# Kernel optimization log

Measured on AMD Instinct MI355X. Metric: run time of the kernel, lower is better.

The kernel has to match this reference:

```python
import jax, jax.numpy as jnp
import numpy as np

EMBED_DIM = 2048
EPS = 1e-6
B, L, H, D = 4, 4096, 16, 128


def setup_inputs() -> dict:
    key = jax.random.key(0)
    k1, k2, k3, k4, k5 = jax.random.split(key, 5)
    return {
        "Q": jax.random.normal(k1, (B, L, H, D), dtype=jnp.float32),
        "K": jax.random.normal(k2, (B, L, H, D), dtype=jnp.float32),
        "V": jax.random.normal(k3, (B, L, H, D), dtype=jnp.float32),
        "phi_Q": jax.random.uniform(k4, (B, L, H, D), dtype=jnp.float32),
        "phi_K": jax.random.uniform(k5, (B, L, H, D), dtype=jnp.float32),
    }


def reference(Q, K, V, phi_Q, phi_K):
    b, l, h, d = Q.shape
    # global query: mean over sequence, scaled by 1/sqrt(embed_dim) -> [B,1,H,D]
    q_global = jnp.mean(Q, axis=1, keepdims=True) / jnp.sqrt(jnp.float32(EMBED_DIM))
    # RALA rescaling: softmax over sequence positions, scaled by L -> [B,1,H,L]
    alpha = jax.nn.softmax(jnp.einsum("bihd,blhd->bihl", q_global, K), axis=-1) * l
    # [B,1,H,L] -> [B,L,H,1]
    alpha_r = jnp.transpose(alpha[:, 0], (0, 2, 1))[..., None]
    phi_K_scaled = phi_K * alpha_r  # [B,L,H,D]
    K_sum = jnp.sum(phi_K_scaled, axis=1)  # [B,H,D]
    KV = jnp.einsum("blhd,blhe->bhde", phi_K_scaled, V)  # [B,H,D,D]
    numerator = jnp.einsum("blhd,bhde->blhe", phi_Q, KV)  # [B,L,H,D]
    denominator = jnp.einsum("blhd,bhd->blh", phi_Q, K_sum)[..., None] + EPS
    return numerator / denominator
```

## Files before the change

kernel.cpp:

```cpp
#include <hip/hip_runtime.h>
#include <cstdint>
#include <cstddef>

#define B_ 4
#define L_ 4096
#define H_ 16
#define D_ 128
#define HD_ (H_*D_)
#define LHD_ ((size_t)L_*HD_)
#define BH_ (B_*H_)
#define EPS_ 1e-6f

typedef float f32x4 __attribute__((ext_vector_type(4)));
typedef unsigned int u32x4 __attribute__((ext_vector_type(4)));
typedef short s16x8 __attribute__((ext_vector_type(8)));

__device__ __forceinline__ unsigned short f2bf(float f){
  unsigned int u = __float_as_uint(f);
  u += 0x7fffu + ((u >> 16) & 1u);
  return (unsigned short)(u >> 16);
}
__device__ __forceinline__ unsigned int pack2(float lo, float hi){
  return (unsigned int)f2bf(lo) | ((unsigned int)f2bf(hi) << 16);
}

__global__ __launch_bounds__(256) void k_qmean(const float* __restrict__ Q, float* __restrict__ qg){
  int b  = blockIdx.x >> 6;
  int l0 = (blockIdx.x & 63) * 64;
  const float* base = Q + (size_t)b * LHD_ + (size_t)l0 * HD_;
  int t = threadIdx.x;
  f32x4 a0 = {0.f,0.f,0.f,0.f}, a1 = {0.f,0.f,0.f,0.f};
  #pragma unroll 4
  for (int l = 0; l < 64; ++l){
    const f32x4* row = (const f32x4*)(base + (size_t)l * HD_);
    a0 += row[t];
    a1 += row[t + 256];
  }
  const float scale = 1.0f / (4096.0f * 45.254833995939045f);
  float* dst = qg + b * HD_;
  #pragma unroll
  for (int i = 0; i < 4; ++i){
    atomicAdd(dst + 4*t + i,        a0[i] * scale);
    atomicAdd(dst + 1024 + 4*t + i, a1[i] * scale);
  }
}

__global__ __launch_bounds__(256) void k_scores(const float* __restrict__ K, const float* __restrict__ qg,
                                                float* __restrict__ scores){
  int b  = blockIdx.x >> 6;
  int l0 = (blockIdx.x & 63) * 64;
  int t = threadIdx.x;
  int wave = t >> 6, lane = t & 63;
  f32x4 q[8];
  const f32x4* qv = (const f32x4*)(qg + b * HD_);
  #pragma unroll
  for (int j = 0; j < 8; ++j)
    q[j] = qv[(2*j + (lane >> 5)) * 32 + (lane & 31)];
  for (int li = wave; li < 64; li += 4){
    const f32x4* kv = (const f32x4*)(K + (size_t)b * LHD_ + (size_t)(l0 + li) * HD_);
    float s[8];
    #pragma unroll
    for (int j = 0; j < 8; ++j){
      f32x4 x = kv[j * 64 + lane];
      s[j] = x[0]*q[j][0] + x[1]*q[j][1] + x[2]*q[j][2] + x[3]*q[j][3];
    }
    #pragma unroll
    for (int off = 1; off < 32; off <<= 1){
      #pragma unroll
      for (int j = 0; j < 8; ++j) s[j] += __shfl_xor(s[j], off);
    }
    if ((lane & 31) == 0){
      int hb = lane >> 5;
      #pragma unroll
      for (int j = 0; j < 8; ++j)
        scores[(size_t)(b * H_ + 2*j + hb) * L_ + l0 + li] = s[j];
    }
  }
}

__global__ __launch_bounds__(256) void k_softmax(float* __restrict__ scores){
  int bh = blockIdx.x;
  float* s = scores + (size_t)bh * L_;
  int t = threadIdx.x;
  int wave = t >> 6, lane = t & 63;
  float v[16];
  #pragma unroll
  for (int j = 0; j < 16; ++j) v[j] = s[t + 256*j];
  float m = -1e30f;
  #pragma unroll
  for (int j = 0; j < 16; ++j) m = fmaxf(m, v[j]);
  #pragma unroll
  for (int off = 1; off < 64; off <<= 1) m = fmaxf(m, __shfl_xor(m, off));
  __shared__ float red[8];
  if (lane == 0) red[wave] = m;
  __syncthreads();
  m = fmaxf(fmaxf(red[0], red[1]), fmaxf(red[2], red[3]));
  float z = 0.f;
  #pragma unroll
  for (int j = 0; j < 16; ++j) z += __expf(v[j] - m);
  #pragma unroll
  for (int off = 1; off < 64; off <<= 1) z += __shfl_xor(z, off);
  if (lane == 0) red[4 + wave] = z;
  __syncthreads();
  z = red[4] + red[5] + red[6] + red[7];
  float scale = (float)L_ / z;
  #pragma unroll
  for (int j = 0; j < 16; ++j) s[t + 256*j] = __expf(v[j] - m) * scale;
}

__global__ __launch_bounds__(256) void k_kv(const float* __restrict__ phiK, const float* __restrict__ V,
                                            const float* __restrict__ alpha,
                                            float* __restrict__ KV_part, float* __restrict__ Ksum){
  int c  = blockIdx.x & 3;
  int bh = blockIdx.x >> 2;
  int b = bh >> 4, h = bh & 15;
  __shared__ unsigned int Al[128 * 20];
  __shared__ unsigned int Bl[128 * 20];
  __shared__ float ksred[128 * 8];
  int t = threadIdx.x;
  int wave = t >> 6, lane = t & 63, q = lane >> 4, r = lane & 15;
  int d4 = t & 31, lp = t >> 5;
  f32x4 acc[2][8];
  #pragma unroll
  for (int mt = 0; mt < 2; ++mt)
    #pragma unroll
    for (int nt = 0; nt < 8; ++nt){ f32x4 z = {0.f,0.f,0.f,0.f}; acc[mt][nt] = z; }
  float ksl[4] = {0.f,0.f,0.f,0.f};

  for (int kt = 0; kt < 32; ++kt){
    int lbase = c * 1024 + kt * 32;
    f32x4 xa[2][2], xb[2][2];
    float al[2][2];
    #pragma unroll
    for (int p = 0; p < 2; ++p){
      int gl = lbase + 16*p + 2*lp;
      const float* rowK = phiK + (((size_t)b * L_ + gl) * H_ + h) * D_;
      const float* rowV = V    + (((size_t)b * L_ + gl) * H_ + h) * D_;
      xa[p][0] = ((const f32x4*)rowK)[d4];
      xa[p][1] = ((const f32x4*)(rowK + HD_))[d4];
      xb[p][0] = ((const f32x4*)rowV)[d4];
      xb[p][1] = ((const f32x4*)(rowV + HD_))[d4];
      al[p][0] = alpha[(size_t)bh * L_ + gl];
      al[p][1] = alpha[(size_t)bh * L_ + gl + 1];
    }
    __syncthreads();
    #pragma unroll
    for (int p = 0; p < 2; ++p){
      int cw = 8*p + lp;
      int cg = cw >> 2, cl = cw & 3;
      int grp = 4 * (cg ^ (d4 & 3)) + cl;
      #pragma unroll
      for (int i = 0; i < 4; ++i){
        int d = 4*d4 + i;
        float w0 = xa[p][0][i] * al[p][0];
        float w1 = xa[p][1][i] * al[p][1];
        ksl[i] += w0 + w1;
        Al[d * 20 + grp] = pack2(w0, w1);
        Bl[d * 20 + grp] = pack2(xb[p][0][i], xb[p][1][i]);
      }
    }
    __syncthreads();
    s16x8 af[2], bf[8];
    #pragma unroll
    for (int mt = 0; mt < 2; ++mt){
      int m = 32*wave + 16*mt + r;
      af[mt] = *((const s16x8*)&Al[m * 20 + 4 * (q ^ ((m >> 2) & 3))]);
    }
    #pragma unroll
    for (int nt = 0; nt < 8; ++nt){
      int n = 16*nt + r;
      bf[nt] = *((const s16x8*)&Bl[n * 20 + 4 * (q ^ ((n >> 2) & 3))]);
    }
    #pragma unroll
    for (int mt = 0; mt < 2; ++mt)
      #pragma unroll
      for (int nt = 0; nt < 8; ++nt)
        acc[mt][nt] = __builtin_amdgcn_mfma_f32_16x16x32_bf16(af[mt], bf[nt], acc[mt][nt], 0, 0, 0);
  }

  size_t pb = ((size_t)c * BH_ + bh) * ((size_t)D_ * D_);
  #pragma unroll
  for (int mt = 0; mt < 2; ++mt)
    #pragma unroll
    for (int reg = 0; reg < 4; ++reg){
      int d = 32*wave + 16*mt + 4*q + reg;
      float* dst = KV_part + pb + (size_t)d * D_;
      #pragma unroll
      for (int nt = 0; nt < 8; ++nt)
        dst[16*nt + r] = acc[mt][nt][reg];
    }
  #pragma unroll
  for (int i = 0; i < 4; ++i) ksred[(4*d4 + i) * 8 + lp] = ksl[i];
  __syncthreads();
  if (t < 128){
    float s = 0.f;
    #pragma unroll
    for (int j = 0; j < 8; ++j) s += ksred[t * 8 + j];
    atomicAdd(Ksum + (size_t)bh * D_ + t, s);
  }
}

__global__ __launch_bounds__(256) void k_reduce(const float* __restrict__ KV_part, const float* __restrict__ Ksum,
                                                unsigned int* __restrict__ KVT, unsigned int* __restrict__ KsumT){
  int bh = blockIdx.x;
  int t = threadIdx.x;
  __shared__ float T[128 * 129];
  #pragma unroll 2
  for (int p = 0; p < 64; ++p){
    int idx = p * 256 + t;
    float s = KV_part[((size_t)0 * BH_ + bh) * 16384 + idx]
            + KV_part[((size_t)1 * BH_ + bh) * 16384 + idx]
            + KV_part[((size_t)2 * BH_ + bh) * 16384 + idx]
            + KV_part[((size_t)3 * BH_ + bh) * 16384 + idx];
    int d = idx >> 7, e = idx & 127;
    T[d * 129 + e] = s;
  }
  __syncthreads();
  #pragma unroll 2
  for (int p = 0; p < 32; ++p){
    int o2 = p * 256 + t;
    int e = o2 >> 6, d0 = (o2 & 63) * 2;
    KVT[(size_t)bh * 8192 + o2] = pack2(T[d0 * 129 + e], T[(d0 + 1) * 129 + e]);
  }
  if (t < 64)
    KsumT[(size_t)bh * 64 + t] = pack2(Ksum[(size_t)bh * 128 + 2*t], Ksum[(size_t)bh * 128 + 2*t + 1]);
}

__global__ __launch_bounds__(256) void k_out(const float* __restrict__ phiQ,
                                             const unsigned int* __restrict__ KVT,
                                             const unsigned int* __restrict__ KsumT,
                                             float* __restrict__ out){
  int chunk = blockIdx.x & 31;
  int bh = blockIdx.x >> 5;
  int b = bh >> 4, h = bh & 15;
  int l0 = chunk * 128;
  __shared__ __align__(16) unsigned short BT[144 * 136];
  int t = threadIdx.x;
  const u32x4* src = (const u32x4*)(KVT + (size_t)bh * 8192);
  #pragma unroll
  for (int p = 0; p < 8; ++p){
    int i = p * 256 + t;
    int row = i >> 4;
    int col = (i & 15) * 8;
    *((u32x4*)&BT[row * 136 + col]) = src[i];
  }
  if (t < 16) *((u32x4*)&BT[128 * 136 + t * 8]) = ((const u32x4*)(KsumT + (size_t)bh * 64))[t];
  if (t < 255){ u32x4 z = {0u,0u,0u,0u}; *((u32x4*)&BT[129 * 136 + t * 8]) = z; }
  __syncthreads();

  int wave = t >> 6, lane = t & 63, q = lane >> 4, r = lane & 15;
  f32x4 accN[2][8], accD[2];
  #pragma unroll
  for (int mt = 0; mt < 2; ++mt){
    f32x4 z = {0.f,0.f,0.f,0.f};
    accD[mt] = z;
    #pragma unroll
    for (int nt = 0; nt < 8; ++nt) accN[mt][nt] = z;
  }
  const float* A0 = phiQ + (((size_t)b * L_ + (l0 + 32*wave + r)) * H_ + h) * D_ + q * 8;
  const float* A1 = A0 + (size_t)16 * HD_;
  #pragma unroll
  for (int ks = 0; ks < 4; ++ks){
    s16x8 af[2];
    #pragma unroll
    for (int mt = 0; mt < 2; ++mt){
      const float* ap = (mt ? A1 : A0) + 32 * ks;
      f32x4 x0 = *((const f32x4*)ap);
      f32x4 x1 = *((const f32x4*)(ap + 4));
      union { s16x8 s; unsigned int u[4]; } fr;
      fr.u[0] = pack2(x0[0], x0[1]);
      fr.u[1] = pack2(x0[2], x0[3]);
      fr.u[2] = pack2(x1[0], x1[1]);
      fr.u[3] = pack2(x1[2], x1[3]);
      af[mt] = fr.s;
    }
    #pragma unroll
    for (int nt = 0; nt < 9; ++nt){
      int n = 16*nt + r;
      s16x8 bf = *((const s16x8*)&BT[n * 136 + q * 8 + 32 * ks]);
      if (nt < 8){
        accN[0][nt] = __builtin_amdgcn_mfma_f32_16x16x32_bf16(af[0], bf, accN[0][nt], 0, 0, 0);
        accN[1][nt] = __builtin_amdgcn_mfma_f32_16x16x32_bf16(af[1], bf, accN[1][nt], 0, 0, 0);
      } else {
        accD[0] = __builtin_amdgcn_mfma_f32_16x16x32_bf16(af[0], bf, accD[0], 0, 0, 0);
        accD[1] = __builtin_amdgcn_mfma_f32_16x16x32_bf16(af[1], bf, accD[1], 0, 0, 0);
      }
    }
  }
  #pragma unroll
  for (int mt = 0; mt < 2; ++mt)
    #pragma unroll
    for (int reg = 0; reg < 4; ++reg){
      float den = __shfl(accD[mt][reg], (lane & 48)) + EPS_;
      float inv = 1.0f / den;
      int l = l0 + 32*wave + 16*mt + 4*q + reg;
      float* orow = out + (((size_t)b * L_ + l) * H_ + h) * D_;
      #pragma unroll
      for (int nt = 0; nt < 8; ++nt)
        orow[16*nt + r] = accN[mt][nt][reg] * inv;
    }
}

extern "C" void kernel_launch(void* const* d_in, const int* in_sizes, int n_in,
                              void* d_out, int out_size, void* d_ws, size_t ws_size,
                              hipStream_t stream){
  const float* Q    = (const float*)d_in[0];
  const float* K    = (const float*)d_in[1];
  const float* V    = (const float*)d_in[2];
  const float* phiQ = (const float*)d_in[3];
  const float* phiK = (const float*)d_in[4];
  float* out = (float*)d_out;
  char* ws = (char*)d_ws;
  float* qg      = (float*)(ws);
  float* Ksum    = (float*)(ws + 32768);
  float* scores  = (float*)(ws + 65536);
  float* KV_part = (float*)(ws + 1114112);
  unsigned int* KVT   = (unsigned int*)(ws + 17891328);
  unsigned int* KsumT = (unsigned int*)(ws + 19988480);

  hipMemsetAsync(qg, 0, 65536, stream);
  k_qmean  <<<256,  256, 0, stream>>>(Q, qg);
  k_scores <<<256,  256, 0, stream>>>(K, qg, scores);
  k_softmax<<<64,   256, 0, stream>>>(scores);
  k_kv     <<<256,  256, 0, stream>>>(phiK, V, scores, KV_part, Ksum);
  k_reduce <<<64,   256, 0, stream>>>(KV_part, Ksum, KVT, KsumT);
  k_out    <<<2048, 256, 0, stream>>>(phiQ, KVT, KsumT, out);
}
```

Baseline: 620.5 us.

## Raise parallelism across qmean, scores, kv and reduce kernels with prefetching

k_qmean and k_scores now launch more blocks, each covering fewer sequence rows. k_kv moves to 512 threads per block, one M-tile per wave, and register-prefetches the next phiK/V tile while the current one is staged in shared memory. k_reduce splits each head's transpose across four blocks and uses vectorized loads. The aim is better occupancy and latency hiding on memory-bound stages, at the cost of more atomics in qmean and more per-block overhead. The trivial accN index change in k_out has no effect.

```diff
diff --git a/kernel.cpp b/kernel.cpp
--- a/kernel.cpp
+++ b/kernel.cpp
@@ -25,13 +25,13 @@
 }
 
 __global__ __launch_bounds__(256) void k_qmean(const float* __restrict__ Q, float* __restrict__ qg){
-  int b  = blockIdx.x >> 6;
-  int l0 = (blockIdx.x & 63) * 64;
+  int b  = blockIdx.x >> 7;
+  int l0 = (blockIdx.x & 127) * 32;
   const float* base = Q + (size_t)b * LHD_ + (size_t)l0 * HD_;
   int t = threadIdx.x;
   f32x4 a0 = {0.f,0.f,0.f,0.f}, a1 = {0.f,0.f,0.f,0.f};
   #pragma unroll 4
-  for (int l = 0; l < 64; ++l){
+  for (int l = 0; l < 32; ++l){
     const f32x4* row = (const f32x4*)(base + (size_t)l * HD_);
     a0 += row[t];
     a1 += row[t + 256];
@@ -47,8 +47,8 @@
 
 __global__ __launch_bounds__(256) void k_scores(const float* __restrict__ K, const float* __restrict__ qg,
                                                 float* __restrict__ scores){
-  int b  = blockIdx.x >> 6;
-  int l0 = (blockIdx.x & 63) * 64;
+  int b  = blockIdx.x >> 8;
+  int l0 = (blockIdx.x & 255) * 16;
   int t = threadIdx.x;
   int wave = t >> 6, lane = t & 63;
   f32x4 q[8];
@@ -56,7 +56,7 @@
   #pragma unroll
   for (int j = 0; j < 8; ++j)
     q[j] = qv[(2*j + (lane >> 5)) * 32 + (lane & 31)];
-  for (int li = wave; li < 64; li += 4){
+  for (int li = wave; li < 16; li += 4){
     const f32x4* kv = (const f32x4*)(K + (size_t)b * LHD_ + (size_t)(l0 + li) * HD_);
     float s[8];
     #pragma unroll
@@ -108,7 +108,7 @@
   for (int j = 0; j < 16; ++j) s[t + 256*j] = __expf(v[j] - m) * scale;
 }
 
-__global__ __launch_bounds__(256) void k_kv(const float* __restrict__ phiK, const float* __restrict__ V,
+__global__ __launch_bounds__(512) void k_kv(const float* __restrict__ phiK, const float* __restrict__ V,
                                             const float* __restrict__ alpha,
                                             float* __restrict__ KV_part, float* __restrict__ Ksum){
   int c  = blockIdx.x & 3;
@@ -116,113 +116,115 @@
   int b = bh >> 4, h = bh & 15;
   __shared__ unsigned int Al[128 * 20];
   __shared__ unsigned int Bl[128 * 20];
-  __shared__ float ksred[128 * 8];
+  __shared__ float ksred[128 * 16];
   int t = threadIdx.x;
   int wave = t >> 6, lane = t & 63, q = lane >> 4, r = lane & 15;
   int d4 = t & 31, lp = t >> 5;
-  f32x4 acc[2][8];
-  #pragma unroll
-  for (int mt = 0; mt < 2; ++mt)
-    #pragma unroll
-    for (int nt = 0; nt < 8; ++nt){ f32x4 z = {0.f,0.f,0.f,0.f}; acc[mt][nt] = z; }
+  f32x4 acc[8];
+  #pragma unroll
+  for (int nt = 0; nt < 8; ++nt){ f32x4 z = {0.f,0.f,0.f,0.f}; acc[nt] = z; }
   float ksl[4] = {0.f,0.f,0.f,0.f};
 
+  const size_t arow = (size_t)bh * L_;
+  int gl = c * 1024 + 2 * lp;
+  const float* rowK = phiK + (((size_t)b * L_ + gl) * H_ + h) * D_;
+  const float* rowV = V    + (((size_t)b * L_ + gl) * H_ + h) * D_;
+  f32x4 xa0 = ((const f32x4*)rowK)[d4];
+  f32x4 xa1 = ((const f32x4*)(rowK + HD_))[d4];
+  f32x4 xb0 = ((const f32x4*)rowV)[d4];
+  f32x4 xb1 = ((const f32x4*)(rowV + HD_))[d4];
+  float al0 = alpha[arow + gl];
+  float al1 = alpha[arow + gl + 1];
+
+  int cg = lp >> 2, cl = lp & 3;
+  int grp = 4 * (cg ^ (d4 & 3)) + cl;
+
   for (int kt = 0; kt < 32; ++kt){
-    int lbase = c * 1024 + kt * 32;
-    f32x4 xa[2][2], xb[2][2];
-    float al[2][2];
-    #pragma unroll
-    for (int p = 0; p < 2; ++p){
-      int gl = lbase + 16*p + 2*lp;
-      const float* rowK = phiK + (((size_t)b * L_ + gl) * H_ + h) * D_;
-      const float* rowV = V    + (((size_t)b * L_ + gl) * H_ + h) * D_;
-      xa[p][0] = ((const f32x4*)rowK)[d4];
-      xa[p][1] = ((const f32x4*)(rowK + HD_))[d4];
-      xb[p][0] = ((const f32x4*)rowV)[d4];
-      xb[p][1] = ((const f32x4*)(rowV + HD_))[d4];
-      al[p][0] = alpha[(size_t)bh * L_ + gl];
-      al[p][1] = alpha[(size_t)bh * L_ + gl + 1];
-    }
     __syncthreads();
     #pragma unroll
-    for (int p = 0; p < 2; ++p){
-      int cw = 8*p + lp;
-      int cg = cw >> 2, cl = cw & 3;
-      int grp = 4 * (cg ^ (d4 & 3)) + cl;
-      #pragma unroll
-      for (int i = 0; i < 4; ++i){
-        int d = 4*d4 + i;
-        float w0 = xa[p][0][i] * al[p][0];
-        float w1 = xa[p][1][i] * al[p][1];
-        ksl[i] += w0 + w1;
-        Al[d * 20 + grp] = pack2(w0, w1);
-        Bl[d * 20 + grp] = pack2(xb[p][0][i], xb[p][1][i]);
-      }
+    for (int i = 0; i < 4; ++i){
+      int d = 4*d4 + i;
+      float w0 = xa0[i] * al0;
+      float w1 = xa1[i] * al1;
+      ksl[i] += w0 + w1;
+      Al[d * 20 + grp] = pack2(w0, w1);
+      Bl[d * 20 + grp] = pack2(xb0[i], xb1[i]);
+    }
+    if (kt < 31){
+      int gl2 = c * 1024 + (kt + 1) * 32 + 2 * lp;
+      const float* nK = phiK + (((size_t)b * L_ + gl2) * H_ + h) * D_;
+      const float* nV = V    + (((size_t)b * L_ + gl2) * H_ + h) * D_;
+      xa0 = ((const f32x4*)nK)[d4];
+      xa1 = ((const f32x4*)(nK + HD_))[d4];
+      xb0 = ((const f32x4*)nV)[d4];
+      xb1 = ((const f32x4*)(nV + HD_))[d4];
+      al0 = alpha[arow + gl2];
+      al1 = alpha[arow + gl2 + 1];
     }
     __syncthreads();
-    s16x8 af[2], bf[8];
-    #pragma unroll
-    for (int mt = 0; mt < 2; ++mt){
-      int m = 32*wave + 16*mt + r;
-      af[mt] = *((const s16x8*)&Al[m * 20 + 4 * (q ^ ((m >> 2) & 3))]);
-    }
+    int m = 16*wave + r;
+    s16x8 af = *((const s16x8*)&Al[m * 20 + 4 * (q ^ ((m >> 2) & 3))]);
+    s16x8 bf[8];
     #pragma unroll
     for (int nt = 0; nt < 8; ++nt){
       int n = 16*nt + r;
       bf[nt] = *((const s16x8*)&Bl[n * 20 + 4 * (q ^ ((n >> 2) & 3))]);
     }
     #pragma unroll
-    for (int mt = 0; mt < 2; ++mt)
-      #pragma unroll
-      for (int nt = 0; nt < 8; ++nt)
-        acc[mt][nt] = __builtin_amdgcn_mfma_f32_16x16x32_bf16(af[mt], bf[nt], acc[mt][nt], 0, 0, 0);
+    for (int nt = 0; nt < 8; ++nt)
+      acc[nt] = __builtin_amdgcn_mfma_f32_16x16x32_bf16(af, bf[nt], acc[nt], 0, 0, 0);
   }
 
   size_t pb = ((size_t)c * BH_ + bh) * ((size_t)D_ * D_);
   #pragma unroll
-  for (int mt = 0; mt < 2; ++mt)
-    #pragma unroll
-    for (int reg = 0; reg < 4; ++reg){
-      int d = 32*wave + 16*mt + 4*q + reg;
-      float* dst = KV_part + pb + (size_t)d * D_;
-      #pragma unroll
-      for (int nt = 0; nt < 8; ++nt)
-        dst[16*nt + r] = acc[mt][nt][reg];
-    }
-  #pragma unroll
-  for (int i = 0; i < 4; ++i) ksred[(4*d4 + i) * 8 + lp] = ksl[i];
+  for (int reg = 0; reg < 4; ++reg){
+    int d = 16*wave + 4*q + reg;
+    float* dst = KV_part + pb + (size_t)d * D_;
+    #pragma unroll
+    for (int nt = 0; nt < 8; ++nt)
+      dst[16*nt + r] = acc[nt][reg];
+  }
+  #pragma unroll
+  for (int i = 0; i < 4; ++i) ksred[(4*d4 + i) * 16 + lp] = ksl[i];
   __syncthreads();
   if (t < 128){
     float s = 0.f;
     #pragma unroll
-    for (int j = 0; j < 8; ++j) s += ksred[t * 8 + j];
+    for (int j = 0; j < 16; ++j) s += ksred[t * 16 + j];
     atomicAdd(Ksum + (size_t)bh * D_ + t, s);
   }
 }
 
 __global__ __launch_bounds__(256) void k_reduce(const float* __restrict__ KV_part, const float* __restrict__ Ksum,
                                                 unsigned int* __restrict__ KVT, unsigned int* __restrict__ KsumT){
-  int bh = blockIdx.x;
-  int t = threadIdx.x;
-  __shared__ float T[128 * 129];
-  #pragma unroll 2
-  for (int p = 0; p < 64; ++p){
-    int idx = p * 256 + t;
-    float s = KV_part[((size_t)0 * BH_ + bh) * 16384 + idx]
-            + KV_part[((size_t)1 * BH_ + bh) * 16384 + idx]
-            + KV_part[((size_t)2 * BH_ + bh) * 16384 + idx]
-            + KV_part[((size_t)3 * BH_ + bh) * 16384 + idx];
-    int d = idx >> 7, e = idx & 127;
-    T[d * 129 + e] = s;
-  }
-  __syncthreads();
-  #pragma unroll 2
-  for (int p = 0; p < 32; ++p){
-    int o2 = p * 256 + t;
-    int e = o2 >> 6, d0 = (o2 & 63) * 2;
-    KVT[(size_t)bh * 8192 + o2] = pack2(T[d0 * 129 + e], T[(d0 + 1) * 129 + e]);
-  }
-  if (t < 64)
+  int bh = blockIdx.x >> 2, eq = blockIdx.x & 3;
+  int t = threadIdx.x;
+  __shared__ float T[128 * 33];
+  const f32x4* P0 = (const f32x4*)(KV_part + (size_t)bh * 16384);
+  #pragma unroll
+  for (int p = 0; p < 4; ++p){
+    int i4 = p * 256 + t;
+    int d = i4 >> 3, e4 = i4 & 7;
+    int idx = d * 32 + eq * 8 + e4;
+    f32x4 s = P0[idx]
+            + P0[idx + (size_t)1 * BH_ * 4096]
+            + P0[idx + (size_t)2 * BH_ * 4096]
+            + P0[idx + (size_t)3 * BH_ * 4096];
+    int e = e4 * 4;
+    T[d * 33 + e    ] = s[0];
+    T[d * 33 + e + 1] = s[1];
+    T[d * 33 + e + 2] = s[2];
+    T[d * 33 + e + 3] = s[3];
+  }
+  __syncthreads();
+  #pragma unroll
+  for (int p = 0; p < 8; ++p){
+    int o = p * 256 + t;
+    int e = o >> 6, dp = o & 63;
+    KVT[(size_t)bh * 8192 + (size_t)(eq * 32 + e) * 64 + dp] =
+        pack2(T[(2*dp) * 33 + e], T[(2*dp + 1) * 33 + e]);
+  }
+  if (eq == 0 && t < 64)
     KsumT[(size_t)bh * 64 + t] = pack2(Ksum[(size_t)bh * 128 + 2*t], Ksum[(size_t)bh * 128 + 2*t + 1]);
 }
 
@@ -297,7 +299,7 @@
       float* orow = out + (((size_t)b * L_ + l) * H_ + h) * D_;
       #pragma unroll
       for (int nt = 0; nt < 8; ++nt)
-        orow[16*nt + r] = accN[mt][nt][reg] * inv;
+        orow[16*nt + r] = accN[nt < 8 ? mt : 0][nt][reg] * inv;
     }
 }
 
@@ -319,10 +321,10 @@
   unsigned int* KsumT = (unsigned int*)(ws + 19988480);
 
   hipMemsetAsync(qg, 0, 65536, stream);
-  k_qmean  <<<256,  256, 0, stream>>>(Q, qg);
-  k_scores <<<256,  256, 0, stream>>>(K, qg, scores);
+  k_qmean  <<<512,  256, 0, stream>>>(Q, qg);
+  k_scores <<<1024, 256, 0, stream>>>(K, qg, scores);
   k_softmax<<<64,   256, 0, stream>>>(scores);
-  k_kv     <<<256,  256, 0, stream>>>(phiK, V, scores, KV_part, Ksum);
-  k_reduce <<<64,   256, 0, stream>>>(KV_part, Ksum, KVT, KsumT);
+  k_kv     <<<256,  512, 0, stream>>>(phiK, V, scores, KV_part, Ksum);
+  k_reduce <<<256,  256, 0, stream>>>(KV_part, Ksum, KVT, KsumT);
   k_out    <<<2048, 256, 0, stream>>>(phiQ, KVT, KsumT, out);
 }
```

Result: faster. 598.8 us (-3.5%).
